# Performance work log

Hardware: AMD Instinct MI355X
Metric: run time of the kernel (lower is better)

The kernel has to match this reference:

```python
import jax, jax.numpy as jnp
import numpy as np

FEATURE_DIM = 128
HIDDEN_DIM = 64
MAPPING_SIZE = 64
SCALE = 10.0
B, N, H, W = 8, 65536, 56, 56


def setup_inputs() -> dict:
    key = jax.random.key(0)
    ks = jax.random.split(key, 12)
    features = jax.random.normal(ks[0], (B, FEATURE_DIM, H, W), dtype=jnp.float32)
    # points in [-1, 1]^3
    points = jax.random.uniform(ks[1], (B, N, 3), dtype=jnp.float32, minval=-1.0, maxval=1.0)
    # realistic pinhole intrinsics for a 56x56 feature map
    k_mat = jnp.array([[56.0, 0.0, 28.0], [0.0, 56.0, 28.0], [0.0, 0.0, 1.0]], dtype=jnp.float32)
    k = jnp.broadcast_to(k_mat, (B, 3, 3))
    # extrinsics: identity rotation, translate z by 2 so points are in front of camera
    rt_mat = jnp.concatenate([jnp.eye(3, dtype=jnp.float32), jnp.array([[0.0], [0.0], [2.0]], dtype=jnp.float32)], axis=1)
    rt = jnp.broadcast_to(rt_mat, (B, 3, 4))
    # learned params
    B_gauss = jax.random.normal(ks[2], (MAPPING_SIZE, 3), dtype=jnp.float32) * SCALE
    input_dim = FEATURE_DIM + 2 * MAPPING_SIZE
    W1 = jax.random.normal(ks[3], (input_dim, HIDDEN_DIM), dtype=jnp.float32) * 0.05
    b1 = jnp.zeros((HIDDEN_DIM,), dtype=jnp.float32)
    W2 = jax.random.normal(ks[4], (HIDDEN_DIM, HIDDEN_DIM), dtype=jnp.float32) * 0.05
    b2 = jnp.zeros((HIDDEN_DIM,), dtype=jnp.float32)
    W3 = jax.random.normal(ks[5], (HIDDEN_DIM, HIDDEN_DIM), dtype=jnp.float32) * 0.05
    b3 = jnp.zeros((HIDDEN_DIM,), dtype=jnp.float32)
    W4 = jax.random.normal(ks[6], (HIDDEN_DIM, 1), dtype=jnp.float32) * 0.05
    b4 = jnp.zeros((1,), dtype=jnp.float32)
    return {"features": features, "points": points, "k": k, "rt": rt,
            "B_gauss": B_gauss, "W1": W1, "b1": b1, "W2": W2, "b2": b2,
            "W3": W3, "b3": b3, "W4": W4, "b4": b4}


def _grid_sample_bilinear_zeros(grid, x, y):
    # grid: (B, C, H, W); x, y: (B, N) pixel coords (align_corners=False already unnormalized)
    Bc, C, Hc, Wc = grid.shape
    g = jnp.transpose(grid, (0, 2, 3, 1))  # (B, H, W, C)
    x0 = jnp.floor(x)
    y0 = jnp.floor(y)
    wx1 = x - x0  # frac
    wy1 = y - y0
    wx0 = 1.0 - wx1
    wy0 = 1.0 - wy1
    x0i = x0.astype(jnp.int32)
    y0i = y0.astype(jnp.int32)
    bidx = jnp.arange(Bc, dtype=jnp.int32)[:, None]  # (B, 1)

    def gather(ix, iy):
        inb = ((ix >= 0) & (ix < Wc) & (iy >= 0) & (iy < Hc)).astype(grid.dtype)  # (B, N)
        vals = g[bidx, jnp.clip(iy, 0, Hc - 1), jnp.clip(ix, 0, Wc - 1)]  # (B, N, C)
        return vals * inb[..., None]

    out = (gather(x0i, y0i) * (wx0 * wy0)[..., None]
           + gather(x0i + 1, y0i) * (wx1 * wy0)[..., None]
           + gather(x0i, y0i + 1) * (wx0 * wy1)[..., None]
           + gather(x0i + 1, y0i + 1) * (wx1 * wy1)[..., None])
    return out  # (B, N, C)


def reference(features, points, k, rt, B_gauss, W1, b1, W2, b2, W3, b3, W4, b4):
    Bc, Nc, _ = points.shape
    Hc, Wc = features.shape[-2:]
    # --- camera projection ---
    homo = jnp.concatenate([points, jnp.ones((Bc, Nc, 1), dtype=points.dtype)], axis=2)  # (B,N,4)
    cam = jnp.einsum('bij,bnj->bni', rt, homo)   # (B,N,3)
    img = jnp.einsum('bij,bnj->bni', k, cam)     # (B,N,3)
    z = img[:, :, 2:3] + 1e-8
    uv = img[:, :, :2] / z
    valid = (img[:, :, 2:3] > 0).astype(points.dtype)  # (B,N,1)
    u_norm = (2.0 * uv[..., 0] + 1.0) / Wc - 1.0
    v_norm = (2.0 * uv[..., 1] + 1.0) / Hc - 1.0
    # grid_sample align_corners=False unnormalization: ix = ((g+1)*W - 1)/2
    x = ((u_norm + 1.0) * Wc - 1.0) * 0.5
    y = ((v_norm + 1.0) * Hc - 1.0) * 0.5
    img_feats = _grid_sample_bilinear_zeros(features, x, y) * valid  # (B,N,C)
    # --- Fourier mapping ---
    x_proj = (2.0 * np.pi) * jnp.einsum('bnd,md->bnm', points, B_gauss)  # (B,N,M)
    coord_feats = jnp.concatenate([jnp.sin(x_proj), jnp.cos(x_proj)], axis=-1)  # (B,N,2M)
    # --- MLP ---
    inp = jnp.concatenate([img_feats, coord_feats], axis=2)  # (B,N,C+2M)
    h = jax.nn.relu(inp @ W1 + b1)
    h = jax.nn.relu(h @ W2 + b2)
    h = jax.nn.relu(h @ W3 + b3)
    out = h @ W4 + b4  # (B,N,1)
    return out
```

## Files before the change

kernel.cpp:

```cpp
#include <hip/hip_runtime.h>

#define FDIM 128
#define HDIM 64
#define MSIZE 64
#define IMG_W 56
#define IMG_H 56
#define NPIX (IMG_W * IMG_H)
#define NB 8
#define NPTS 65536

typedef _Float16 f16x8 __attribute__((ext_vector_type(8)));
typedef float f32x4 __attribute__((ext_vector_type(4)));
typedef int i32x4 __attribute__((ext_vector_type(4)));

#define W2_OFF 16384
#define W3_OFF 20480
#define FT_BYTE_OFF 49152

__device__ __forceinline__ void lds_fence() {
    __asm__ volatile("s_waitcnt lgkmcnt(0)" ::: "memory");
}

__global__ __launch_bounds__(256) void transpose_feats16(const float* __restrict__ in,
                                                         _Float16* __restrict__ out) {
    __shared__ float tile[64][129];
    const int b = blockIdx.y;
    const int pbase = blockIdx.x * 64;
    const int t = threadIdx.x;
    const float* src = in + (size_t)b * FDIM * NPIX;
    _Float16*    dst = out + (size_t)b * NPIX * FDIM;
    const int tx = t & 63;
    const int cg = t >> 6;
#pragma unroll
    for (int i = 0; i < 32; ++i) {
        int c = cg * 32 + i;
        tile[tx][c] = src[(size_t)c * NPIX + pbase + tx];
    }
    __syncthreads();
    const int sub = t >> 4;
    const int hk  = (t & 15) * 8;
#pragma unroll
    for (int g = 0; g < 4; ++g) {
        const int px = g * 16 + sub;
        f16x8 hv;
#pragma unroll
        for (int j = 0; j < 8; ++j) hv[j] = (_Float16)tile[px][hk + j];
        *(f16x8*)(dst + (size_t)(pbase + px) * FDIM + hk) = hv;
    }
}

__global__ __launch_bounds__(256) void pack_weights(const float* __restrict__ W1,
                                                    const float* __restrict__ W2,
                                                    const float* __restrict__ W3,
                                                    _Float16* __restrict__ ws) {
    const int t = blockIdx.x * 256 + threadIdx.x;
    if (t >= 3072) return;
    const int l = t & 63;
    const int q = l >> 4;
    const int col = l & 15;
    const int frag = t >> 6;
    if (frag < 32) {
        const int kt = frag >> 2, nt = frag & 3;
#pragma unroll
        for (int j = 0; j < 8; ++j) {
            int k = kt * 32 + q * 8 + j;
            int row = (k < 128) ? k : (128 + (k & 1) * 64 + ((k - 128) >> 1));
            ws[((size_t)(frag * 64 + l)) * 8 + j] = (_Float16)W1[row * HDIM + nt * 16 + col];
        }
    } else if (frag < 40) {
        const int f2 = frag - 32;
        const int kt = f2 >> 2, nt = f2 & 3;
#pragma unroll
        for (int j = 0; j < 8; ++j) {
            int row = kt * 32 + q * 8 + j;
            ws[W2_OFF + ((size_t)(f2 * 64 + l)) * 8 + j] = (_Float16)W2[row * HDIM + nt * 16 + col];
        }
    } else {
        const int f3 = frag - 40;
        const int kt = f3 >> 2, nt = f3 & 3;
#pragma unroll
        for (int j = 0; j < 8; ++j) {
            int row = kt * 32 + q * 8 + j;
            ws[W3_OFF + ((size_t)(f3 * 64 + l)) * 8 + j] = (_Float16)W3[row * HDIM + nt * 16 + col];
        }
    }
}

__global__ __launch_bounds__(256, 2) void decoder_mfma2(
    const _Float16* __restrict__ ft,
    const float* __restrict__ points,
    const float* __restrict__ Kmat, const float* __restrict__ Rt,
    const float* __restrict__ Bg,
    const _Float16* __restrict__ wfrag,
    const float* __restrict__ b1, const float* __restrict__ b2,
    const float* __restrict__ b3,
    const float* __restrict__ W4, const float* __restrict__ b4,
    float* __restrict__ out) {
    __shared__ _Float16 lds[4 * 64 * 72];
    const int tid = threadIdx.x;
    const int wid = tid >> 6;
    const int l   = tid & 63;
    const int q   = l >> 4;
    const int col = l & 15;
    const int b    = blockIdx.x >> 8;
    const int base = blockIdx.x * 256 + wid * 64;
    const int gid  = base + l;
    _Float16* Ah = lds + wid * 64 * 72;
    float* sh = (float*)Ah;
    int*   shi = (int*)Ah;

    const float px = points[(size_t)gid * 3 + 0];
    const float py = points[(size_t)gid * 3 + 1];
    const float pz = points[(size_t)gid * 3 + 2];
    const float* rt = Rt + b * 12;
    const float* km = Kmat + b * 9;
    float cx = rt[0] * px + rt[1] * py + rt[2]  * pz + rt[3];
    float cy = rt[4] * px + rt[5] * py + rt[6]  * pz + rt[7];
    float cz = rt[8] * px + rt[9] * py + rt[10] * pz + rt[11];
    float ix = km[0] * cx + km[1] * cy + km[2] * cz;
    float iy = km[3] * cx + km[4] * cy + km[5] * cz;
    float iz = km[6] * cx + km[7] * cy + km[8] * cz;
    float z  = iz + 1e-8f;
    float u  = ix / z;
    float v  = iy / z;
    float valid = (iz > 0.0f) ? 1.0f : 0.0f;
    float u_norm = (2.0f * u + 1.0f) / (float)IMG_W - 1.0f;
    float v_norm = (2.0f * v + 1.0f) / (float)IMG_H - 1.0f;
    float x = ((u_norm + 1.0f) * (float)IMG_W - 1.0f) * 0.5f;
    float y = ((v_norm + 1.0f) * (float)IMG_H - 1.0f) * 0.5f;
    float x0f = floorf(x), y0f = floorf(y);
    float wx1 = x - x0f, wy1 = y - y0f;
    float wx0 = 1.0f - wx1, wy0 = 1.0f - wy1;
    int x0 = (int)x0f, y0 = (int)y0f;
    int x1 = x0 + 1, y1 = y0 + 1;
    int x0c = x0 < 0 ? 0 : (x0 > IMG_W - 1 ? IMG_W - 1 : x0);
    int x1c = x1 < 0 ? 0 : (x1 > IMG_W - 1 ? IMG_W - 1 : x1);
    int y0c = y0 < 0 ? 0 : (y0 > IMG_H - 1 ? IMG_H - 1 : y0);
    int y1c = y1 < 0 ? 0 : (y1 > IMG_H - 1 ? IMG_H - 1 : y1);
    float mx0 = (x0 >= 0 && x0 < IMG_W) ? 1.0f : 0.0f;
    float mx1 = (x1 >= 0 && x1 < IMG_W) ? 1.0f : 0.0f;
    float my0 = (y0 >= 0 && y0 < IMG_H) ? 1.0f : 0.0f;
    float my1 = (y1 >= 0 && y1 < IMG_H) ? 1.0f : 0.0f;
    const int pb = b * NPIX;
    sh[l * 12 + 0] = wx0 * wy0 * mx0 * my0 * valid;
    sh[l * 12 + 1] = wx1 * wy0 * mx1 * my0 * valid;
    sh[l * 12 + 2] = wx0 * wy1 * mx0 * my1 * valid;
    sh[l * 12 + 3] = wx1 * wy1 * mx1 * my1 * valid;
    shi[l * 12 + 4] = (pb + y0c * IMG_W + x0c) * FDIM;
    shi[l * 12 + 5] = (pb + y0c * IMG_W + x1c) * FDIM;
    shi[l * 12 + 6] = (pb + y1c * IMG_W + x0c) * FDIM;
    shi[l * 12 + 7] = (pb + y1c * IMG_W + x1c) * FDIM;
    sh[l * 12 + 8]  = px;
    sh[l * 12 + 9]  = py;
    sh[l * 12 + 10] = pz;
    lds_fence();

    const f32x4 zero4 = {0.0f, 0.0f, 0.0f, 0.0f};
    f32x4 acc[4][4];
#pragma unroll
    for (int mt = 0; mt < 4; ++mt)
#pragma unroll
        for (int nt = 0; nt < 4; ++nt) acc[mt][nt] = zero4;

#pragma unroll
    for (int mt = 0; mt < 4; ++mt) {
        const float* e = sh + (mt * 16 + col) * 12;
        f32x4 wv = *(const f32x4*)(e);
        i32x4 iv = *(const i32x4*)(e + 4);
        float qx = e[8], qy = e[9], qz = e[10];
#pragma unroll
        for (int ktg = 0; ktg < 4; ++ktg) {
            const int co = ktg * 32 + q * 8;
            f16x8 v00 = *(const f16x8*)(ft + iv.x + co);
            f16x8 v10 = *(const f16x8*)(ft + iv.y + co);
            f16x8 v01 = *(const f16x8*)(ft + iv.z + co);
            f16x8 v11 = *(const f16x8*)(ft + iv.w + co);
            f16x8 af;
#pragma unroll
            for (int j = 0; j < 8; ++j) {
                float r = wv.x * (float)v00[j] + wv.y * (float)v10[j]
                        + wv.z * (float)v01[j] + wv.w * (float)v11[j];
                af[j] = (_Float16)r;
            }
#pragma unroll
            for (int nt = 0; nt < 4; ++nt) {
                f16x8 bf = *(const f16x8*)(wfrag + ((size_t)((ktg * 4 + nt) * 64 + l)) * 8);
                acc[mt][nt] = __builtin_amdgcn_mfma_f32_16x16x32_f16(af, bf, acc[mt][nt], 0, 0, 0);
            }
        }
#pragma unroll
        for (int ktf = 0; ktf < 4; ++ktf) {
            f16x8 af;
#pragma unroll
            for (int i = 0; i < 4; ++i) {
                const int m = ktf * 16 + q * 4 + i;
                float t = Bg[m * 3 + 0] * qx + Bg[m * 3 + 1] * qy + Bg[m * 3 + 2] * qz;
                float tf = t - floorf(t);
                af[2 * i]     = (_Float16)__builtin_amdgcn_sinf(tf);
                af[2 * i + 1] = (_Float16)__builtin_amdgcn_cosf(tf);
            }
#pragma unroll
            for (int nt = 0; nt < 4; ++nt) {
                f16x8 bf = *(const f16x8*)(wfrag + ((size_t)(((4 + ktf) * 4 + nt) * 64 + l)) * 8);
                acc[mt][nt] = __builtin_amdgcn_mfma_f32_16x16x32_f16(af, bf, acc[mt][nt], 0, 0, 0);
            }
        }
    }

    float bb[4];
#pragma unroll
    for (int nt = 0; nt < 4; ++nt) bb[nt] = b1[nt * 16 + col];
#pragma unroll
    for (int mt = 0; mt < 4; ++mt)
#pragma unroll
        for (int nt = 0; nt < 4; ++nt)
#pragma unroll
            for (int r = 0; r < 4; ++r) {
                float hv = fmaxf(acc[mt][nt][r] + bb[nt], 0.0f);
                Ah[(mt * 16 + q * 4 + r) * 72 + nt * 16 + col] = (_Float16)hv;
            }
    lds_fence();

#pragma unroll
    for (int mt = 0; mt < 4; ++mt)
#pragma unroll
        for (int nt = 0; nt < 4; ++nt) acc[mt][nt] = zero4;
#pragma unroll
    for (int ktl = 0; ktl < 2; ++ktl) {
        f16x8 bf[4];
#pragma unroll
        for (int nt = 0; nt < 4; ++nt)
            bf[nt] = *(const f16x8*)(wfrag + W2_OFF + ((size_t)((ktl * 4 + nt) * 64 + l)) * 8);
#pragma unroll
        for (int mt = 0; mt < 4; ++mt) {
            f16x8 af = *(const f16x8*)(&Ah[(mt * 16 + col) * 72 + ktl * 32 + q * 8]);
#pragma unroll
            for (int nt = 0; nt < 4; ++nt)
                acc[mt][nt] = __builtin_amdgcn_mfma_f32_16x16x32_f16(af, bf[nt], acc[mt][nt], 0, 0, 0);
        }
    }
    lds_fence();
#pragma unroll
    for (int nt = 0; nt < 4; ++nt) bb[nt] = b2[nt * 16 + col];
#pragma unroll
    for (int mt = 0; mt < 4; ++mt)
#pragma unroll
        for (int nt = 0; nt < 4; ++nt)
#pragma unroll
            for (int r = 0; r < 4; ++r) {
                float hv = fmaxf(acc[mt][nt][r] + bb[nt], 0.0f);
                Ah[(mt * 16 + q * 4 + r) * 72 + nt * 16 + col] = (_Float16)hv;
            }
    lds_fence();

#pragma unroll
    for (int mt = 0; mt < 4; ++mt)
#pragma unroll
        for (int nt = 0; nt < 4; ++nt) acc[mt][nt] = zero4;
#pragma unroll
    for (int ktl = 0; ktl < 2; ++ktl) {
        f16x8 bf[4];
#pragma unroll
        for (int nt = 0; nt < 4; ++nt)
            bf[nt] = *(const f16x8*)(wfrag + W3_OFF + ((size_t)((ktl * 4 + nt) * 64 + l)) * 8);
#pragma unroll
        for (int mt = 0; mt < 4; ++mt) {
            f16x8 af = *(const f16x8*)(&Ah[(mt * 16 + col) * 72 + ktl * 32 + q * 8]);
#pragma unroll
            for (int nt = 0; nt < 4; ++nt)
                acc[mt][nt] = __builtin_amdgcn_mfma_f32_16x16x32_f16(af, bf[nt], acc[mt][nt], 0, 0, 0);
        }
    }

    float b3v[4], w4v[4];
#pragma unroll
    for (int nt = 0; nt < 4; ++nt) {
        b3v[nt] = b3[nt * 16 + col];
        w4v[nt] = W4[nt * 16 + col];
    }
    const float b4v = b4[0];
#pragma unroll
    for (int mt = 0; mt < 4; ++mt)
#pragma unroll
        for (int r = 0; r < 4; ++r) {
            float p = 0.0f;
#pragma unroll
            for (int nt = 0; nt < 4; ++nt)
                p = fmaf(fmaxf(acc[mt][nt][r] + b3v[nt], 0.0f), w4v[nt], p);
            p += __shfl_xor(p, 1);
            p += __shfl_xor(p, 2);
            p += __shfl_xor(p, 4);
            p += __shfl_xor(p, 8);
            if (col == 0) out[base + mt * 16 + q * 4 + r] = p + b4v;
        }
}

__global__ __launch_bounds__(64, 2) void decoder_valu(
    const float* __restrict__ feats, const float* __restrict__ points,
    const float* __restrict__ Kmat, const float* __restrict__ Rt,
    const float* __restrict__ Bg,
    const float* __restrict__ W1, const float* __restrict__ b1,
    const float* __restrict__ W2, const float* __restrict__ b2,
    const float* __restrict__ W3, const float* __restrict__ b3,
    const float* __restrict__ W4, const float* __restrict__ b4,
    float* __restrict__ out) {
    __shared__ float hbuf[64 * 65];
    const int tid = threadIdx.x;
    const int b   = blockIdx.x / (NPTS / 64);
    const int gid = blockIdx.x * 64 + tid;
    const float px = points[(size_t)gid * 3 + 0];
    const float py = points[(size_t)gid * 3 + 1];
    const float pz = points[(size_t)gid * 3 + 2];
    const float* rt = Rt + b * 12;
    const float* km = Kmat + b * 9;
    float cx = rt[0] * px + rt[1] * py + rt[2]  * pz + rt[3];
    float cy = rt[4] * px + rt[5] * py + rt[6]  * pz + rt[7];
    float cz = rt[8] * px + rt[9] * py + rt[10] * pz + rt[11];
    float ix = km[0] * cx + km[1] * cy + km[2] * cz;
    float iy = km[3] * cx + km[4] * cy + km[5] * cz;
    float iz = km[6] * cx + km[7] * cy + km[8] * cz;
    float z  = iz + 1e-8f;
    float u  = ix / z, v = iy / z;
    float valid = (iz > 0.0f) ? 1.0f : 0.0f;
    float u_norm = (2.0f * u + 1.0f) / (float)IMG_W - 1.0f;
    float v_norm = (2.0f * v + 1.0f) / (float)IMG_H - 1.0f;
    float x = ((u_norm + 1.0f) * (float)IMG_W - 1.0f) * 0.5f;
    float y = ((v_norm + 1.0f) * (float)IMG_H - 1.0f) * 0.5f;
    float x0f = floorf(x), y0f = floorf(y);
    float wx1 = x - x0f, wy1 = y - y0f;
    float wx0 = 1.0f - wx1, wy0 = 1.0f - wy1;
    int x0 = (int)x0f, y0 = (int)y0f;
    int x1 = x0 + 1, y1 = y0 + 1;
    int x0c = x0 < 0 ? 0 : (x0 > IMG_W - 1 ? IMG_W - 1 : x0);
    int x1c = x1 < 0 ? 0 : (x1 > IMG_W - 1 ? IMG_W - 1 : x1);
    int y0c = y0 < 0 ? 0 : (y0 > IMG_H - 1 ? IMG_H - 1 : y0);
    int y1c = y1 < 0 ? 0 : (y1 > IMG_H - 1 ? IMG_H - 1 : y1);
    float mx0 = (x0 >= 0 && x0 < IMG_W) ? 1.0f : 0.0f;
    float mx1 = (x1 >= 0 && x1 < IMG_W) ? 1.0f : 0.0f;
    float my0 = (y0 >= 0 && y0 < IMG_H) ? 1.0f : 0.0f;
    float my1 = (y1 >= 0 && y1 < IMG_H) ? 1.0f : 0.0f;
    float w00 = wx0 * wy0 * mx0 * my0 * valid;
    float w10 = wx1 * wy0 * mx1 * my0 * valid;
    float w01 = wx0 * wy1 * mx0 * my1 * valid;
    float w11 = wx1 * wy1 * mx1 * my1 * valid;
    float h[HDIM];
#pragma unroll
    for (int j = 0; j < HDIM; ++j) h[j] = b1[j];
    const float* fb = feats + (size_t)b * FDIM * NPIX;
    const int p00 = y0c * IMG_W + x0c, p10 = y0c * IMG_W + x1c;
    const int p01 = y1c * IMG_W + x0c, p11 = y1c * IMG_W + x1c;
#pragma unroll 1
    for (int c = 0; c < FDIM; ++c) {
        const float* fp = fb + (size_t)c * NPIX;
        float fv = w00 * fp[p00] + w10 * fp[p10] + w01 * fp[p01] + w11 * fp[p11];
        const float* wr = W1 + (size_t)c * HDIM;
#pragma unroll
        for (int j = 0; j < HDIM; ++j) h[j] = fmaf(fv, wr[j], h[j]);
    }
#pragma unroll 1
    for (int m = 0; m < MSIZE; ++m) {
        float t = Bg[m * 3 + 0] * px + Bg[m * 3 + 1] * py + Bg[m * 3 + 2] * pz;
        float tf = t - floorf(t);
        float s = __builtin_amdgcn_sinf(tf);
        float c = __builtin_amdgcn_cosf(tf);
        const float* wsn = W1 + (size_t)(FDIM + m) * HDIM;
        const float* wcs = W1 + (size_t)(FDIM + MSIZE + m) * HDIM;
#pragma unroll
        for (int j = 0; j < HDIM; ++j)
            h[j] = fmaf(s, wsn[j], fmaf(c, wcs[j], h[j]));
    }
    float* myh = &hbuf[tid * 65];
#pragma unroll
    for (int j = 0; j < HDIM; ++j) myh[j] = fmaxf(h[j], 0.0f);
    float h2[HDIM];
#pragma unroll
    for (int j = 0; j < HDIM; ++j) h2[j] = b2[j];
#pragma unroll 1
    for (int i = 0; i < HDIM; ++i) {
        float hi = myh[i];
        const float* wr = W2 + (size_t)i * HDIM;
#pragma unroll
        for (int j = 0; j < HDIM; ++j) h2[j] = fmaf(hi, wr[j], h2[j]);
    }
#pragma unroll
    for (int j = 0; j < HDIM; ++j) myh[j] = fmaxf(h2[j], 0.0f);
#pragma unroll
    for (int j = 0; j < HDIM; ++j) h[j] = b3[j];
#pragma unroll 1
    for (int i = 0; i < HDIM; ++i) {
        float hi = myh[i];
        const float* wr = W3 + (size_t)i * HDIM;
#pragma unroll
        for (int j = 0; j < HDIM; ++j) h[j] = fmaf(hi, wr[j], h[j]);
    }
    float acc = b4[0];
#pragma unroll
    for (int j = 0; j < HDIM; ++j) acc = fmaf(fmaxf(h[j], 0.0f), W4[j], acc);
    out[gid] = acc;
}

extern "C" void kernel_launch(void* const* d_in, const int* in_sizes, int n_in,
                              void* d_out, int out_size, void* d_ws, size_t ws_size,
                              hipStream_t stream) {
    const float* feats = (const float*)d_in[0];
    const float* pts   = (const float*)d_in[1];
    const float* k     = (const float*)d_in[2];
    const float* rt    = (const float*)d_in[3];
    const float* Bg    = (const float*)d_in[4];
    const float* W1    = (const float*)d_in[5];
    const float* b1    = (const float*)d_in[6];
    const float* W2    = (const float*)d_in[7];
    const float* b2    = (const float*)d_in[8];
    const float* W3    = (const float*)d_in[9];
    const float* b3    = (const float*)d_in[10];
    const float* W4    = (const float*)d_in[11];
    const float* b4    = (const float*)d_in[12];
    float* out = (float*)d_out;

    const size_t ftBytes = (size_t)NB * NPIX * FDIM * sizeof(_Float16);

    if (ws_size >= FT_BYTE_OFF + ftBytes) {
        _Float16* wf = (_Float16*)d_ws;
        _Float16* ft = (_Float16*)((char*)d_ws + FT_BYTE_OFF);
        pack_weights<<<12, 256, 0, stream>>>(W1, W2, W3, wf);
        transpose_feats16<<<dim3(NPIX / 64, NB), 256, 0, stream>>>(feats, ft);
        decoder_mfma2<<<NB * NPTS / 256, 256, 0, stream>>>(ft, pts, k, rt, Bg, wf,
                                                           b1, b2, b3, W4, b4, out);
    } else {
        decoder_valu<<<NB * NPTS / 64, 64, 0, stream>>>(feats, pts, k, rt, Bg,
                                                        W1, b1, W2, b2, W3, b3, W4, b4, out);
    }
}
```

Measured before the change: 186.6 us.

## Fuse prep kernels, interleave batches across blocks, prefetch gathers and use fp16 bilinear

Merges the feature-transpose and weight-pack launches into one prep kernel, cutting one launch. Decoder blocks now interleave batch indices so neighbouring blocks read different feature maps. The Fourier-feature MFMAs run first with hoisted Bg and weight-fragment loads. The bilinear gather is software-pipelined by prefetching the next channel group, and the interpolation is done in packed fp16 instead of fp32, which costs some accuracy.

```diff
diff --git a/kernel.cpp b/kernel.cpp
--- a/kernel.cpp
+++ b/kernel.cpp
@@ -16,72 +16,73 @@
 #define W2_OFF 16384
 #define W3_OFF 20480
 #define FT_BYTE_OFF 49152
+#define TR_BLOCKS (NPIX / 64 * NB)
 
 __device__ __forceinline__ void lds_fence() {
     __asm__ volatile("s_waitcnt lgkmcnt(0)" ::: "memory");
 }
 
-__global__ __launch_bounds__(256) void transpose_feats16(const float* __restrict__ in,
-                                                         _Float16* __restrict__ out) {
-    __shared__ float tile[64][129];
-    const int b = blockIdx.y;
-    const int pbase = blockIdx.x * 64;
-    const int t = threadIdx.x;
-    const float* src = in + (size_t)b * FDIM * NPIX;
-    _Float16*    dst = out + (size_t)b * NPIX * FDIM;
-    const int tx = t & 63;
-    const int cg = t >> 6;
-#pragma unroll
-    for (int i = 0; i < 32; ++i) {
-        int c = cg * 32 + i;
-        tile[tx][c] = src[(size_t)c * NPIX + pbase + tx];
-    }
-    __syncthreads();
-    const int sub = t >> 4;
-    const int hk  = (t & 15) * 8;
-#pragma unroll
-    for (int g = 0; g < 4; ++g) {
-        const int px = g * 16 + sub;
-        f16x8 hv;
-#pragma unroll
-        for (int j = 0; j < 8; ++j) hv[j] = (_Float16)tile[px][hk + j];
-        *(f16x8*)(dst + (size_t)(pbase + px) * FDIM + hk) = hv;
-    }
-}
-
-__global__ __launch_bounds__(256) void pack_weights(const float* __restrict__ W1,
-                                                    const float* __restrict__ W2,
-                                                    const float* __restrict__ W3,
-                                                    _Float16* __restrict__ ws) {
-    const int t = blockIdx.x * 256 + threadIdx.x;
-    if (t >= 3072) return;
-    const int l = t & 63;
-    const int q = l >> 4;
-    const int col = l & 15;
-    const int frag = t >> 6;
-    if (frag < 32) {
-        const int kt = frag >> 2, nt = frag & 3;
-#pragma unroll
-        for (int j = 0; j < 8; ++j) {
-            int k = kt * 32 + q * 8 + j;
-            int row = (k < 128) ? k : (128 + (k & 1) * 64 + ((k - 128) >> 1));
-            ws[((size_t)(frag * 64 + l)) * 8 + j] = (_Float16)W1[row * HDIM + nt * 16 + col];
-        }
-    } else if (frag < 40) {
-        const int f2 = frag - 32;
-        const int kt = f2 >> 2, nt = f2 & 3;
-#pragma unroll
-        for (int j = 0; j < 8; ++j) {
-            int row = kt * 32 + q * 8 + j;
-            ws[W2_OFF + ((size_t)(f2 * 64 + l)) * 8 + j] = (_Float16)W2[row * HDIM + nt * 16 + col];
+__global__ __launch_bounds__(256) void prep_kernel(const float* __restrict__ in,
+                                                   const float* __restrict__ W1,
+                                                   const float* __restrict__ W2,
+                                                   const float* __restrict__ W3,
+                                                   _Float16* __restrict__ ws) {
+    if (blockIdx.x < TR_BLOCKS) {
+        __shared__ float tile[64][129];
+        _Float16* out = ws + FT_BYTE_OFF / 2;
+        const int b = blockIdx.x / (NPIX / 64);
+        const int pbase = (blockIdx.x % (NPIX / 64)) * 64;
+        const int t = threadIdx.x;
+        const float* src = in + (size_t)b * FDIM * NPIX;
+        _Float16*    dst = out + (size_t)b * NPIX * FDIM;
+        const int tx = t & 63;
+        const int cg = t >> 6;
+#pragma unroll
+        for (int i = 0; i < 32; ++i) {
+            int c = cg * 32 + i;
+            tile[tx][c] = src[(size_t)c * NPIX + pbase + tx];
+        }
+        __syncthreads();
+        const int sub = t >> 4;
+        const int hk  = (t & 15) * 8;
+#pragma unroll
+        for (int g = 0; g < 4; ++g) {
+            const int px = g * 16 + sub;
+            f16x8 hv;
+#pragma unroll
+            for (int j = 0; j < 8; ++j) hv[j] = (_Float16)tile[px][hk + j];
+            *(f16x8*)(dst + (size_t)(pbase + px) * FDIM + hk) = hv;
         }
     } else {
-        const int f3 = frag - 40;
-        const int kt = f3 >> 2, nt = f3 & 3;
-#pragma unroll
-        for (int j = 0; j < 8; ++j) {
-            int row = kt * 32 + q * 8 + j;
-            ws[W3_OFF + ((size_t)(f3 * 64 + l)) * 8 + j] = (_Float16)W3[row * HDIM + nt * 16 + col];
+        const int t = (blockIdx.x - TR_BLOCKS) * 256 + threadIdx.x;
+        const int l = t & 63;
+        const int q = l >> 4;
+        const int col = l & 15;
+        const int frag = t >> 6;
+        if (frag < 32) {
+            const int kt = frag >> 2, nt = frag & 3;
+#pragma unroll
+            for (int j = 0; j < 8; ++j) {
+                int k = kt * 32 + q * 8 + j;
+                int row = (k < 128) ? k : (128 + (k & 1) * 64 + ((k - 128) >> 1));
+                ws[((size_t)(frag * 64 + l)) * 8 + j] = (_Float16)W1[row * HDIM + nt * 16 + col];
+            }
+        } else if (frag < 40) {
+            const int f2 = frag - 32;
+            const int kt = f2 >> 2, nt = f2 & 3;
+#pragma unroll
+            for (int j = 0; j < 8; ++j) {
+                int row = kt * 32 + q * 8 + j;
+                ws[W2_OFF + ((size_t)(f2 * 64 + l)) * 8 + j] = (_Float16)W2[row * HDIM + nt * 16 + col];
+            }
+        } else {
+            const int f3 = frag - 40;
+            const int kt = f3 >> 2, nt = f3 & 3;
+#pragma unroll
+            for (int j = 0; j < 8; ++j) {
+                int row = kt * 32 + q * 8 + j;
+                ws[W3_OFF + ((size_t)(f3 * 64 + l)) * 8 + j] = (_Float16)W3[row * HDIM + nt * 16 + col];
+            }
         }
     }
 }
@@ -102,8 +103,9 @@
     const int l   = tid & 63;
     const int q   = l >> 4;
     const int col = l & 15;
-    const int b    = blockIdx.x >> 8;
-    const int base = blockIdx.x * 256 + wid * 64;
+    const int b    = blockIdx.x & 7;
+    const int grp  = blockIdx.x >> 3;
+    const int base = b * NPTS + grp * 256 + wid * 64;
     const int gid  = base + l;
     _Float16* Ah = lds + wid * 64 * 72;
     float* sh = (float*)Ah;
@@ -162,48 +164,73 @@
 #pragma unroll
         for (int nt = 0; nt < 4; ++nt) acc[mt][nt] = zero4;
 
+    f32x4 wv[4];
+    i32x4 iv[4];
+    float qx[4], qy[4], qz[4];
 #pragma unroll
     for (int mt = 0; mt < 4; ++mt) {
         const float* e = sh + (mt * 16 + col) * 12;
-        f32x4 wv = *(const f32x4*)(e);
-        i32x4 iv = *(const i32x4*)(e + 4);
-        float qx = e[8], qy = e[9], qz = e[10];
+        wv[mt] = *(const f32x4*)(e);
+        iv[mt] = *(const i32x4*)(e + 4);
+        qx[mt] = e[8]; qy[mt] = e[9]; qz[mt] = e[10];
+    }
+
+#pragma unroll
+    for (int ktf = 0; ktf < 4; ++ktf) {
+        float bgx[4], bgy[4], bgz[4];
+#pragma unroll
+        for (int i = 0; i < 4; ++i) {
+            const int m = ktf * 16 + q * 4 + i;
+            bgx[i] = Bg[m * 3 + 0];
+            bgy[i] = Bg[m * 3 + 1];
+            bgz[i] = Bg[m * 3 + 2];
+        }
+        f16x8 bf[4];
+#pragma unroll
+        for (int nt = 0; nt < 4; ++nt)
+            bf[nt] = *(const f16x8*)(wfrag + ((size_t)(((4 + ktf) * 4 + nt) * 64 + l)) * 8);
+#pragma unroll
+        for (int mt = 0; mt < 4; ++mt) {
+            f16x8 af;
+#pragma unroll
+            for (int i = 0; i < 4; ++i) {
+                float t = bgx[i] * qx[mt] + bgy[i] * qy[mt] + bgz[i] * qz[mt];
+                float tf = t - floorf(t);
+                af[2 * i]     = (_Float16)__builtin_amdgcn_sinf(tf);
+                af[2 * i + 1] = (_Float16)__builtin_amdgcn_cosf(tf);
+            }
+#pragma unroll
+            for (int nt = 0; nt < 4; ++nt)
+                acc[mt][nt] = __builtin_amdgcn_mfma_f32_16x16x32_f16(af, bf[nt], acc[mt][nt], 0, 0, 0);
+        }
+    }
+
+#pragma unroll
+    for (int mt = 0; mt < 4; ++mt) {
+        const _Float16 w0h = (_Float16)wv[mt].x, w1h = (_Float16)wv[mt].y;
+        const _Float16 w2h = (_Float16)wv[mt].z, w3h = (_Float16)wv[mt].w;
+        const int co0 = q * 8;
+        f16x8 c00 = *(const f16x8*)(ft + iv[mt].x + co0);
+        f16x8 c10 = *(const f16x8*)(ft + iv[mt].y + co0);
+        f16x8 c01 = *(const f16x8*)(ft + iv[mt].z + co0);
+        f16x8 c11 = *(const f16x8*)(ft + iv[mt].w + co0);
 #pragma unroll
         for (int ktg = 0; ktg < 4; ++ktg) {
-            const int co = ktg * 32 + q * 8;
-            f16x8 v00 = *(const f16x8*)(ft + iv.x + co);
-            f16x8 v10 = *(const f16x8*)(ft + iv.y + co);
-            f16x8 v01 = *(const f16x8*)(ft + iv.z + co);
-            f16x8 v11 = *(const f16x8*)(ft + iv.w + co);
-            f16x8 af;
-#pragma unroll
-            for (int j = 0; j < 8; ++j) {
-                float r = wv.x * (float)v00[j] + wv.y * (float)v10[j]
-                        + wv.z * (float)v01[j] + wv.w * (float)v11[j];
-                af[j] = (_Float16)r;
-            }
+            f16x8 n00, n10, n01, n11;
+            if (ktg < 3) {
+                const int co = (ktg + 1) * 32 + q * 8;
+                n00 = *(const f16x8*)(ft + iv[mt].x + co);
+                n10 = *(const f16x8*)(ft + iv[mt].y + co);
+                n01 = *(const f16x8*)(ft + iv[mt].z + co);
+                n11 = *(const f16x8*)(ft + iv[mt].w + co);
+            }
+            f16x8 af = c00 * w0h + c10 * w1h + c01 * w2h + c11 * w3h;
 #pragma unroll
             for (int nt = 0; nt < 4; ++nt) {
                 f16x8 bf = *(const f16x8*)(wfrag + ((size_t)((ktg * 4 + nt) * 64 + l)) * 8);
                 acc[mt][nt] = __builtin_amdgcn_mfma_f32_16x16x32_f16(af, bf, acc[mt][nt], 0, 0, 0);
             }
-        }
-#pragma unroll
-        for (int ktf = 0; ktf < 4; ++ktf) {
-            f16x8 af;
-#pragma unroll
-            for (int i = 0; i < 4; ++i) {
-                const int m = ktf * 16 + q * 4 + i;
-                float t = Bg[m * 3 + 0] * qx + Bg[m * 3 + 1] * qy + Bg[m * 3 + 2] * qz;
-                float tf = t - floorf(t);
-                af[2 * i]     = (_Float16)__builtin_amdgcn_sinf(tf);
-                af[2 * i + 1] = (_Float16)__builtin_amdgcn_cosf(tf);
-            }
-#pragma unroll
-            for (int nt = 0; nt < 4; ++nt) {
-                f16x8 bf = *(const f16x8*)(wfrag + ((size_t)(((4 + ktf) * 4 + nt) * 64 + l)) * 8);
-                acc[mt][nt] = __builtin_amdgcn_mfma_f32_16x16x32_f16(af, bf, acc[mt][nt], 0, 0, 0);
-            }
+            c00 = n00; c10 = n10; c01 = n01; c11 = n11;
         }
     }
 
@@ -422,8 +449,7 @@
     if (ws_size >= FT_BYTE_OFF + ftBytes) {
         _Float16* wf = (_Float16*)d_ws;
         _Float16* ft = (_Float16*)((char*)d_ws + FT_BYTE_OFF);
-        pack_weights<<<12, 256, 0, stream>>>(W1, W2, W3, wf);
-        transpose_feats16<<<dim3(NPIX / 64, NB), 256, 0, stream>>>(feats, ft);
+        prep_kernel<<<TR_BLOCKS + 12, 256, 0, stream>>>(feats, W1, W2, W3, wf);
         decoder_mfma2<<<NB * NPTS / 256, 256, 0, stream>>>(ft, pts, k, rt, Bg, wf,
                                                            b1, b2, b3, W4, b4, out);
     } else {
```

Result: no change. 184.1 us (-1.3%).
